# Kernel tuning notes

Measured on AMD Instinct MI355X. Metric: run time of the kernel, lower is better.

The kernel has to match this reference:

```python
import jax, jax.numpy as jnp
import numpy as np

B1, B2, N, D = 1, 128, 256, 256
H, C = 8, 32
OUT = 256


def setup_inputs() -> dict:
    key = jax.random.key(0)
    ks = jax.random.split(key, 8)
    in_data = jax.random.normal(ks[0], (B1, B2, N, D), dtype=jnp.float32)
    # binary mask, mostly unmasked
    mask = (jax.random.uniform(ks[1], (B1, B2, N)) > 0.1).astype(jnp.float32)
    nonbatched_bias = jax.random.normal(ks[2], (B1, H, N, N), dtype=jnp.float32)
    scale = 1.0 / np.sqrt(D)
    w_qkv = jax.random.normal(ks[3], (3 * H * C, D), dtype=jnp.float32) * scale  # torch Linear [out,in]
    w_gate = jax.random.normal(ks[4], (H * C, D), dtype=jnp.float32) * scale
    gating_bias = jnp.ones((H * C,), dtype=jnp.float32)
    w_o = jax.random.normal(ks[5], (OUT, H * C), dtype=jnp.float32) * scale
    b_o = jnp.zeros((OUT,), dtype=jnp.float32)
    return {
        "in_data": in_data,
        "mask": mask,
        "nonbatched_bias": nonbatched_bias,
        "w_qkv": w_qkv,
        "w_gate": w_gate,
        "gating_bias": gating_bias,
        "w_o": w_o,
        "b_o": b_o,
    }


def reference(in_data, mask, nonbatched_bias, w_qkv, w_gate, gating_bias, w_o, b_o):
    scaling = C ** (-0.5)
    # fused QKV projection (no bias): [b1,b2,n, 3*h*c]
    qkv = jnp.einsum("xynd,ed->xyne", in_data, w_qkv)
    q, k, v = jnp.split(qkv, 3, axis=-1)

    def heads(t):  # [b1,b2,n,h*c] -> [b1,b2,h,n,c]
        return t.reshape(B1, B2, N, H, C).transpose(0, 1, 3, 2, 4)

    q, k, v = heads(q) * scaling, heads(k), heads(v)
    logits = jnp.einsum("xyhqc,xyhkc->xyhqk", q, k)
    mask_bias = (1e9 * (mask - 1.0))[:, :, None, None, :]  # [b1,b2,1,1,n]
    logits = logits + mask_bias + nonbatched_bias[:, None]  # [b1,b2,h,q,k]
    weights = jax.nn.softmax(logits, axis=-1)
    wa = jnp.einsum("xyhqk,xyhkc->xyhqc", weights, v)
    wa = wa.transpose(0, 1, 3, 2, 4).reshape(B1, B2, N, H * C)
    # sigmoid gating: sigmoid(gate_linear(x) + gating_bias) * weighted_avg
    gate = jax.nn.sigmoid(jnp.einsum("xynd,ed->xyne", in_data, w_gate) + gating_bias)
    wa = gate * wa
    out = jnp.einsum("xyne,oe->xyno", wa, w_o) + b_o
    return out
```

## Files before the change

### kernel.cpp

```cpp
#include <hip/hip_runtime.h>
#include <stdint.h>

#define B2 128
#define NSEQ 256
#define DIM 256
#define NH 8
#define CH 32

typedef __attribute__((ext_vector_type(8))) __bf16 bf16x8;
typedef __attribute__((ext_vector_type(8))) unsigned short u16x8;
typedef __attribute__((ext_vector_type(4))) unsigned short u16x4;
typedef __attribute__((ext_vector_type(4))) float f32x4;

__device__ __forceinline__ unsigned short f2bf(float f) {
  unsigned int u = __builtin_bit_cast(unsigned int, f);
  u += 0x7FFFu + ((u >> 16) & 1u);
  return (unsigned short)(u >> 16);
}
__device__ __forceinline__ float bf2f(unsigned short h) {
  unsigned int u = ((unsigned int)h) << 16;
  return __builtin_bit_cast(float, u);
}
__device__ __forceinline__ bf16x8 as_bf(u16x8 v) { return __builtin_bit_cast(bf16x8, v); }

__device__ __forceinline__ void gload16(void* lds, const void* g) {
  __builtin_amdgcn_global_load_lds(
      (__attribute__((address_space(1))) void*)(g),
      (__attribute__((address_space(3))) void*)(lds), 16, 0, 0);
}

__global__ void k_convert(const float* __restrict__ x, const float* __restrict__ wqkv,
                          const float* __restrict__ wgate, const float* __restrict__ wo,
                          unsigned short* __restrict__ xb, unsigned short* __restrict__ wallb,
                          unsigned short* __restrict__ wob) {
  const int NX = 8388608, NWALL = 262144, NWO = 65536;
  int i = blockIdx.x * blockDim.x + threadIdx.x;
  int total4 = (NX + NWALL + NWO) >> 2;
  if (i >= total4) return;
  int e = i << 2;
  float4 v;
  unsigned short* dst;
  if (e < NX) {
    v = *reinterpret_cast<const float4*>(x + e);
    dst = xb + e;
  } else if (e < NX + NWALL) {
    int o = e - NX;
    v = (o < 196608) ? *reinterpret_cast<const float4*>(wqkv + o)
                     : *reinterpret_cast<const float4*>(wgate + (o - 196608));
    dst = wallb + o;
  } else {
    int o = e - NX - NWALL;
    v = *reinterpret_cast<const float4*>(wo + o);
    dst = wob + o;
  }
  u16x4 r;
  r[0] = f2bf(v.x); r[1] = f2bf(v.y); r[2] = f2bf(v.z); r[3] = f2bf(v.w);
  *reinterpret_cast<u16x4*>(dst) = r;
}

template <int MODE>
__launch_bounds__(256, 4)
__global__ void k_gemm(const unsigned short* __restrict__ A, const unsigned short* __restrict__ Bw,
                       unsigned short* __restrict__ qs, unsigned short* __restrict__ ksb,
                       unsigned short* __restrict__ vsb, unsigned short* __restrict__ gateb,
                       const float* __restrict__ gbias,
                       float* __restrict__ outp, const float* __restrict__ bo) {
  __shared__ __attribute__((aligned(16))) unsigned short As[2][4096];
  __shared__ __attribute__((aligned(16))) unsigned short Bs[2][4096];
  const int tid = threadIdx.x, lane = tid & 63, w = tid >> 6;
  const int wr = w >> 1, wc = w & 1;
  const int l15 = lane & 15, hi = lane >> 4;
  const int m0 = blockIdx.x * 128, n0 = blockIdx.y * 128;

  auto stage = [&](unsigned short* sbuf, const unsigned short* gsrc, int row0, int k0) {
#pragma unroll
    for (int q2 = 0; q2 < 2; ++q2) {
      int ob = (w * 2 + q2) * 1024 + (lane << 4);
      int r = ob >> 6, cb = ob & 63;
      int scb = cb ^ ((r & 3) << 4);
      const unsigned short* g = gsrc + (size_t)(row0 + r) * 256 + k0 + (scb >> 1);
      gload16(sbuf + (size_t)(w * 2 + q2) * 512, g);
    }
  };

  f32x4 acc[4][4];
#pragma unroll
  for (int i = 0; i < 4; ++i) {
#pragma unroll
    for (int j = 0; j < 4; ++j) acc[i][j] = (f32x4){0.f, 0.f, 0.f, 0.f};
  }

  stage(As[0], A, m0, 0);
  stage(Bs[0], Bw, n0, 0);
  asm volatile("s_waitcnt vmcnt(0)" ::: "memory");
  __syncthreads();

#pragma unroll
  for (int kt = 0; kt < 8; ++kt) {
    const int cur = kt & 1;
    if (kt < 7) {
      stage(As[cur ^ 1], A, m0, (kt + 1) * 32);
      stage(Bs[cur ^ 1], Bw, n0, (kt + 1) * 32);
    }
    {
      bf16x8 af[4], bfv[4];
      const int cbx = hi << 4;
#pragma unroll
      for (int fr = 0; fr < 4; ++fr) {
        int ra = wr * 64 + fr * 16 + l15;
        int off = ra * 64 + (cbx ^ ((ra & 3) << 4));
        af[fr] = *reinterpret_cast<const bf16x8*>((const char*)As[cur] + off);
      }
#pragma unroll
      for (int fc = 0; fc < 4; ++fc) {
        int rb = wc * 64 + fc * 16 + l15;
        int off = rb * 64 + (cbx ^ ((rb & 3) << 4));
        bfv[fc] = *reinterpret_cast<const bf16x8*>((const char*)Bs[cur] + off);
      }
#pragma unroll
      for (int fr = 0; fr < 4; ++fr) {
#pragma unroll
        for (int fc = 0; fc < 4; ++fc)
          acc[fr][fc] = __builtin_amdgcn_mfma_f32_16x16x32_bf16(af[fr], bfv[fc], acc[fr][fc], 0, 0, 0);
      }
    }
    asm volatile("s_waitcnt vmcnt(0)" ::: "memory");
    __syncthreads();
  }

  if (MODE == 0) {
#pragma unroll
    for (int fr = 0; fr < 4; ++fr) {
      int mrow = m0 + wr * 64 + fr * 16 + (hi << 2);
      int b = mrow >> 8, n = mrow & 255;
#pragma unroll
      for (int fc = 0; fc < 4; ++fc) {
        int e = n0 + wc * 64 + fc * 16 + l15;
        int which = e >> 8, loc = e & 255, hh = loc >> 5, cc = loc & 31;
#pragma unroll
        for (int i = 0; i < 4; ++i) {
          float v = acc[fr][fc][i];
          size_t idx = ((size_t)(b * 8 + hh) * 256 + (n + i)) * 32 + cc;
          if (which == 0) {
            qs[idx] = f2bf(v * 0.17677669529663687f);
          } else if (which == 1) {
            ksb[idx] = f2bf(v);
          } else if (which == 2) {
            vsb[idx] = f2bf(v);
          } else {
            float gsig = 1.0f / (1.0f + __expf(-(v + gbias[loc])));
            gateb[idx] = f2bf(gsig);
          }
        }
      }
    }
  } else {
#pragma unroll
    for (int fr = 0; fr < 4; ++fr) {
      int mrow = m0 + wr * 64 + fr * 16 + (hi << 2);
#pragma unroll
      for (int fc = 0; fc < 4; ++fc) {
        int e = n0 + wc * 64 + fc * 16 + l15;
        float bb = bo[e];
#pragma unroll
        for (int i = 0; i < 4; ++i)
          outp[(size_t)(mrow + i) * 256 + e] = acc[fr][fc][i] + bb;
      }
    }
  }
}

__launch_bounds__(256, 3)
__global__ void k_attn(const unsigned short* __restrict__ qs, const unsigned short* __restrict__ ksb,
                       const unsigned short* __restrict__ vsb, const unsigned short* __restrict__ gateb,
                       const float* __restrict__ mask, const float* __restrict__ nb,
                       unsigned short* __restrict__ wag) {
  __shared__ __attribute__((aligned(16))) unsigned short vt[32][264];
  __shared__ __attribute__((aligned(16))) unsigned short pch[4][16][72];
  __shared__ __attribute__((aligned(16))) unsigned short Kl[16][64][8];
  __shared__ __attribute__((aligned(16))) float mb[256];
  __shared__ float invl[4][16];
  const int tid = threadIdx.x, lane = tid & 63, w = tid >> 6;
  const int l15 = lane & 15, hi = lane >> 4;
  const int b = blockIdx.x, h = blockIdx.y, qz = blockIdx.z;
  const size_t bh = (size_t)(b * 8 + h);
  const unsigned short* kbase = ksb + bh * 8192;
  const unsigned short* vbase = vsb + bh * 8192;
  const unsigned short* qbase = qs + bh * 8192;
  const float* nbh = nb + (size_t)h * 65536;

  mb[tid] = 1e9f * (mask[b * 256 + tid] - 1.0f);
  {
    const unsigned short* vrow = vbase + tid * 32;
#pragma unroll
    for (int c0 = 0; c0 < 32; c0 += 8) {
      u16x8 vv = *reinterpret_cast<const u16x8*>(vrow + c0);
#pragma unroll
      for (int j = 0; j < 8; ++j) vt[c0 + j][tid] = vv[j];
    }
    const unsigned short* krow = kbase + tid * 32;
#pragma unroll
    for (int c8 = 0; c8 < 4; ++c8)
      *reinterpret_cast<u16x8*>(&Kl[tid >> 4][c8 * 16 + (tid & 15)][0]) =
          *reinterpret_cast<const u16x8*>(krow + c8 * 8);
  }
  __syncthreads();

  const f32x4 zero = {0.f, 0.f, 0.f, 0.f};
#pragma unroll 1
  for (int fr = 0; fr < 2; ++fr) {
    const int q0 = qz * 128 + w * 32 + fr * 16;
    u16x8 qf = *reinterpret_cast<const u16x8*>(qbase + (q0 + l15) * 32 + hi * 8);

    f32x4 sacc[16];
    __builtin_amdgcn_s_setprio(1);
#pragma unroll
    for (int kt = 0; kt < 16; ++kt) {
      bf16x8 kf = *reinterpret_cast<const bf16x8*>(&Kl[kt][lane][0]);
      sacc[kt] = __builtin_amdgcn_mfma_f32_16x16x32_bf16(kf, as_bf(qf), zero, 0, 0, 0);
    }
    __builtin_amdgcn_s_setprio(0);

    const float* nbq = nbh + (size_t)(q0 + l15) * 256;
#pragma unroll
    for (int kt = 0; kt < 16; ++kt) {
      float4 nb4 = *reinterpret_cast<const float4*>(nbq + kt * 16 + hi * 4);
      float4 mb4 = *reinterpret_cast<const float4*>(&mb[kt * 16 + hi * 4]);
      sacc[kt][0] += mb4.x + nb4.x;
      sacc[kt][1] += mb4.y + nb4.y;
      sacc[kt][2] += mb4.z + nb4.z;
      sacc[kt][3] += mb4.w + nb4.w;
    }
    float mx = -3.0e38f;
#pragma unroll
    for (int kt = 0; kt < 16; ++kt) {
#pragma unroll
      for (int i = 0; i < 4; ++i) mx = fmaxf(mx, sacc[kt][i]);
    }
    mx = fmaxf(mx, __shfl_xor(mx, 16));
    mx = fmaxf(mx, __shfl_xor(mx, 32));

    float sum = 0.f;
    f32x4 wacc[2];
    wacc[0] = zero; wacc[1] = zero;
#pragma unroll
    for (int c = 0; c < 4; ++c) {
#pragma unroll
      for (int ktl = 0; ktl < 4; ++ktl) {
        const int kt = c * 4 + ktl;
        u16x4 pv;
#pragma unroll
        for (int i = 0; i < 4; ++i) {
          float p = __expf(sacc[kt][i] - mx);
          sum += p;
          pv[i] = f2bf(p);
        }
        *reinterpret_cast<u16x4*>(&pch[w][l15][ktl * 16 + hi * 4]) = pv;
      }
      asm volatile("s_waitcnt lgkmcnt(0)" ::: "memory");
      __builtin_amdgcn_sched_barrier(0);
      __builtin_amdgcn_s_setprio(1);
#pragma unroll
      for (int ks2 = 0; ks2 < 2; ++ks2) {
        bf16x8 pa = *reinterpret_cast<const bf16x8*>(&pch[w][l15][ks2 * 32 + hi * 8]);
#pragma unroll
        for (int ct = 0; ct < 2; ++ct) {
          bf16x8 vb = *reinterpret_cast<const bf16x8*>(&vt[ct * 16 + l15][c * 64 + ks2 * 32 + hi * 8]);
          wacc[ct] = __builtin_amdgcn_mfma_f32_16x16x32_bf16(pa, vb, wacc[ct], 0, 0, 0);
        }
      }
      __builtin_amdgcn_s_setprio(0);
    }
    sum += __shfl_xor(sum, 16);
    sum += __shfl_xor(sum, 32);
    const float inv = 1.0f / sum;
    if (hi == 0) invl[w][l15] = inv;

    float* et = reinterpret_cast<float*>(&pch[w][0][0]);
#pragma unroll
    for (int ct = 0; ct < 2; ++ct) {
#pragma unroll
      for (int i = 0; i < 4; ++i)
        et[(hi * 4 + i) * 36 + ct * 16 + l15] = wacc[ct][i];
    }
    asm volatile("s_waitcnt lgkmcnt(0)" ::: "memory");
    __builtin_amdgcn_sched_barrier(0);
    const int eq = lane >> 2, eh = lane & 3;
    float4 v0 = *reinterpret_cast<const float4*>(&et[eq * 36 + eh * 8]);
    float4 v1 = *reinterpret_cast<const float4*>(&et[eq * 36 + eh * 8 + 4]);
    const float iv = invl[w][eq];
    const int qrow = q0 + eq;
    u16x8 g = *reinterpret_cast<const u16x8*>(gateb + bh * 8192 + qrow * 32 + eh * 8);
    u16x8 ov;
    ov[0] = f2bf(bf2f(g[0]) * v0.x * iv);
    ov[1] = f2bf(bf2f(g[1]) * v0.y * iv);
    ov[2] = f2bf(bf2f(g[2]) * v0.z * iv);
    ov[3] = f2bf(bf2f(g[3]) * v0.w * iv);
    ov[4] = f2bf(bf2f(g[4]) * v1.x * iv);
    ov[5] = f2bf(bf2f(g[5]) * v1.y * iv);
    ov[6] = f2bf(bf2f(g[6]) * v1.z * iv);
    ov[7] = f2bf(bf2f(g[7]) * v1.w * iv);
    *reinterpret_cast<u16x8*>(wag + ((size_t)(b * 256 + qrow)) * 256 + h * 32 + eh * 8) = ov;
    asm volatile("s_waitcnt lgkmcnt(0)" ::: "memory");
    __builtin_amdgcn_sched_barrier(0);
  }
}

extern "C" void kernel_launch(void* const* d_in, const int* in_sizes, int n_in,
                              void* d_out, int out_size, void* d_ws, size_t ws_size,
                              hipStream_t stream) {
  const float* x     = (const float*)d_in[0];
  const float* mask  = (const float*)d_in[1];
  const float* nb    = (const float*)d_in[2];
  const float* wqkv  = (const float*)d_in[3];
  const float* wgate = (const float*)d_in[4];
  const float* gbias = (const float*)d_in[5];
  const float* wo    = (const float*)d_in[6];
  const float* bo    = (const float*)d_in[7];
  float* outp = (float*)d_out;

  char* ws = (char*)d_ws;
  unsigned short* xb    = (unsigned short*)(ws);
  unsigned short* wallb = (unsigned short*)(ws + 16777216);
  unsigned short* wob   = (unsigned short*)(ws + 17301504);
  unsigned short* qs    = (unsigned short*)(ws + 17432576);
  unsigned short* ksb   = (unsigned short*)(ws + 34209792);
  unsigned short* vsb   = (unsigned short*)(ws + 50987008);
  unsigned short* gateb = (unsigned short*)(ws + 67764224);
  unsigned short* wag   = xb;

  k_convert<<<dim3(8512), dim3(256), 0, stream>>>(x, wqkv, wgate, wo, xb, wallb, wob);
  k_gemm<0><<<dim3(256, 8), dim3(256), 0, stream>>>(xb, wallb, qs, ksb, vsb, gateb, gbias, nullptr, nullptr);
  k_attn<<<dim3(128, 8, 2), dim3(256), 0, stream>>>(qs, ksb, vsb, gateb, mask, nb, wag);
  k_gemm<1><<<dim3(256, 2), dim3(256), 0, stream>>>(wag, wob, nullptr, nullptr, nullptr, nullptr, nullptr, outp, bo);
}
```

Measured before the change: 132.7 us.

## Fuse fp32-to-bf16 input conversion into QKV GEMM and merge attention query halves

The QKV/gate GEMM now stages fp32 activations directly into LDS and converts them to bf16 with packed cvt instructions while building fragments. This removes the separate conversion pass over the 8M-element input, which cost one full read and one write. The attention kernel now uses 512-thread blocks that cover all 256 queries of a (batch, head) pair, so K and V are loaded and transposed once instead of twice. In exchange the GEMM reads twice the bytes per A tile, uses more LDS (occupancy hint lowered to 3), and attention blocks are larger with fewer of them.

```diff
diff --git a/kernel.cpp b/kernel.cpp
--- a/kernel.cpp
+++ b/kernel.cpp
@@ -10,6 +10,7 @@
 typedef __attribute__((ext_vector_type(8))) __bf16 bf16x8;
 typedef __attribute__((ext_vector_type(8))) unsigned short u16x8;
 typedef __attribute__((ext_vector_type(4))) unsigned short u16x4;
+typedef __attribute__((ext_vector_type(4))) unsigned int u32x4;
 typedef __attribute__((ext_vector_type(4))) float f32x4;
 
 __device__ __forceinline__ unsigned short f2bf(float f) {
@@ -22,6 +23,11 @@
   return __builtin_bit_cast(float, u);
 }
 __device__ __forceinline__ bf16x8 as_bf(u16x8 v) { return __builtin_bit_cast(bf16x8, v); }
+__device__ __forceinline__ unsigned int cvtpk(float lo, float hi) {
+  unsigned int r;
+  asm("v_cvt_pk_bf16_f32 %0, %1, %2" : "=v"(r) : "v"(lo), "v"(hi));
+  return r;
+}
 
 __device__ __forceinline__ void gload16(void* lds, const void* g) {
   __builtin_amdgcn_global_load_lds(
@@ -29,27 +35,22 @@
       (__attribute__((address_space(3))) void*)(lds), 16, 0, 0);
 }
 
-__global__ void k_convert(const float* __restrict__ x, const float* __restrict__ wqkv,
-                          const float* __restrict__ wgate, const float* __restrict__ wo,
-                          unsigned short* __restrict__ xb, unsigned short* __restrict__ wallb,
-                          unsigned short* __restrict__ wob) {
-  const int NX = 8388608, NWALL = 262144, NWO = 65536;
+__global__ void k_convert(const float* __restrict__ wqkv, const float* __restrict__ wgate,
+                          const float* __restrict__ wo,
+                          unsigned short* __restrict__ wallb, unsigned short* __restrict__ wob) {
+  const int NWALL = 262144, NWO = 65536;
   int i = blockIdx.x * blockDim.x + threadIdx.x;
-  int total4 = (NX + NWALL + NWO) >> 2;
+  int total4 = (NWALL + NWO) >> 2;
   if (i >= total4) return;
   int e = i << 2;
   float4 v;
   unsigned short* dst;
-  if (e < NX) {
-    v = *reinterpret_cast<const float4*>(x + e);
-    dst = xb + e;
-  } else if (e < NX + NWALL) {
-    int o = e - NX;
-    v = (o < 196608) ? *reinterpret_cast<const float4*>(wqkv + o)
-                     : *reinterpret_cast<const float4*>(wgate + (o - 196608));
-    dst = wallb + o;
+  if (e < NWALL) {
+    v = (e < 196608) ? *reinterpret_cast<const float4*>(wqkv + e)
+                     : *reinterpret_cast<const float4*>(wgate + (e - 196608));
+    dst = wallb + e;
   } else {
-    int o = e - NX - NWALL;
+    int o = e - NWALL;
     v = *reinterpret_cast<const float4*>(wo + o);
     dst = wob + o;
   }
@@ -59,27 +60,49 @@
 }
 
 template <int MODE>
-__launch_bounds__(256, 4)
-__global__ void k_gemm(const unsigned short* __restrict__ A, const unsigned short* __restrict__ Bw,
+__launch_bounds__(256, MODE == 0 ? 3 : 4)
+__global__ void k_gemm(const float* __restrict__ Af, const unsigned short* __restrict__ Ab,
+                       const unsigned short* __restrict__ Bw,
                        unsigned short* __restrict__ qs, unsigned short* __restrict__ ksb,
                        unsigned short* __restrict__ vsb, unsigned short* __restrict__ gateb,
                        const float* __restrict__ gbias,
                        float* __restrict__ outp, const float* __restrict__ bo) {
-  __shared__ __attribute__((aligned(16))) unsigned short As[2][4096];
+  __shared__ __attribute__((aligned(16))) char As[2][MODE == 0 ? 16384 : 8192];
   __shared__ __attribute__((aligned(16))) unsigned short Bs[2][4096];
   const int tid = threadIdx.x, lane = tid & 63, w = tid >> 6;
   const int wr = w >> 1, wc = w & 1;
   const int l15 = lane & 15, hi = lane >> 4;
   const int m0 = blockIdx.x * 128, n0 = blockIdx.y * 128;
 
-  auto stage = [&](unsigned short* sbuf, const unsigned short* gsrc, int row0, int k0) {
+  auto stageA = [&](int buf, int k0) {
+    if constexpr (MODE == 0) {
+#pragma unroll
+      for (int q2 = 0; q2 < 4; ++q2) {
+        int ob = (w * 4 + q2) * 1024 + (lane << 4);
+        int r = ob >> 7, cb = ob & 127;
+        int scb = cb ^ ((r & 7) << 4);
+        const float* g = Af + (size_t)(m0 + r) * 256 + k0 + (scb >> 2);
+        gload16(As[buf] + (size_t)(w * 4 + q2) * 1024, g);
+      }
+    } else {
+#pragma unroll
+      for (int q2 = 0; q2 < 2; ++q2) {
+        int ob = (w * 2 + q2) * 1024 + (lane << 4);
+        int r = ob >> 6, cb = ob & 63;
+        int scb = cb ^ ((r & 3) << 4);
+        const unsigned short* g = Ab + (size_t)(m0 + r) * 256 + k0 + (scb >> 1);
+        gload16(As[buf] + (size_t)(w * 2 + q2) * 1024, g);
+      }
+    }
+  };
+  auto stageB = [&](int buf, int k0) {
 #pragma unroll
     for (int q2 = 0; q2 < 2; ++q2) {
       int ob = (w * 2 + q2) * 1024 + (lane << 4);
       int r = ob >> 6, cb = ob & 63;
       int scb = cb ^ ((r & 3) << 4);
-      const unsigned short* g = gsrc + (size_t)(row0 + r) * 256 + k0 + (scb >> 1);
-      gload16(sbuf + (size_t)(w * 2 + q2) * 512, g);
+      const unsigned short* g = Bw + (size_t)(n0 + r) * 256 + k0 + (scb >> 1);
+      gload16((char*)Bs[buf] + (size_t)(w * 2 + q2) * 1024, g);
     }
   };
 
@@ -90,8 +113,8 @@
     for (int j = 0; j < 4; ++j) acc[i][j] = (f32x4){0.f, 0.f, 0.f, 0.f};
   }
 
-  stage(As[0], A, m0, 0);
-  stage(Bs[0], Bw, n0, 0);
+  stageA(0, 0);
+  stageB(0, 0);
   asm volatile("s_waitcnt vmcnt(0)" ::: "memory");
   __syncthreads();
 
@@ -99,22 +122,34 @@
   for (int kt = 0; kt < 8; ++kt) {
     const int cur = kt & 1;
     if (kt < 7) {
-      stage(As[cur ^ 1], A, m0, (kt + 1) * 32);
-      stage(Bs[cur ^ 1], Bw, n0, (kt + 1) * 32);
+      stageA(cur ^ 1, (kt + 1) * 32);
+      stageB(cur ^ 1, (kt + 1) * 32);
     }
     {
       bf16x8 af[4], bfv[4];
-      const int cbx = hi << 4;
 #pragma unroll
       for (int fr = 0; fr < 4; ++fr) {
         int ra = wr * 64 + fr * 16 + l15;
-        int off = ra * 64 + (cbx ^ ((ra & 3) << 4));
-        af[fr] = *reinterpret_cast<const bf16x8*>((const char*)As[cur] + off);
+        if constexpr (MODE == 0) {
+          const char* base = As[cur] + ra * 128;
+          int sw = (ra & 7) << 4;
+          f32x4 a0 = *reinterpret_cast<const f32x4*>(base + ((hi * 32) ^ sw));
+          f32x4 a1 = *reinterpret_cast<const f32x4*>(base + ((hi * 32 + 16) ^ sw));
+          u32x4 afu;
+          afu[0] = cvtpk(a0[0], a0[1]);
+          afu[1] = cvtpk(a0[2], a0[3]);
+          afu[2] = cvtpk(a1[0], a1[1]);
+          afu[3] = cvtpk(a1[2], a1[3]);
+          af[fr] = __builtin_bit_cast(bf16x8, afu);
+        } else {
+          int off = ra * 64 + ((hi << 4) ^ ((ra & 3) << 4));
+          af[fr] = *reinterpret_cast<const bf16x8*>(As[cur] + off);
+        }
       }
 #pragma unroll
       for (int fc = 0; fc < 4; ++fc) {
         int rb = wc * 64 + fc * 16 + l15;
-        int off = rb * 64 + (cbx ^ ((rb & 3) << 4));
+        int off = rb * 64 + ((hi << 4) ^ ((rb & 3) << 4));
         bfv[fc] = *reinterpret_cast<const bf16x8*>((const char*)Bs[cur] + off);
       }
 #pragma unroll
@@ -170,27 +205,27 @@
   }
 }
 
-__launch_bounds__(256, 3)
+__launch_bounds__(512, 6)
 __global__ void k_attn(const unsigned short* __restrict__ qs, const unsigned short* __restrict__ ksb,
                        const unsigned short* __restrict__ vsb, const unsigned short* __restrict__ gateb,
                        const float* __restrict__ mask, const float* __restrict__ nb,
                        unsigned short* __restrict__ wag) {
   __shared__ __attribute__((aligned(16))) unsigned short vt[32][264];
-  __shared__ __attribute__((aligned(16))) unsigned short pch[4][16][72];
+  __shared__ __attribute__((aligned(16))) unsigned short pch[8][16][72];
   __shared__ __attribute__((aligned(16))) unsigned short Kl[16][64][8];
   __shared__ __attribute__((aligned(16))) float mb[256];
-  __shared__ float invl[4][16];
+  __shared__ float invl[8][16];
   const int tid = threadIdx.x, lane = tid & 63, w = tid >> 6;
   const int l15 = lane & 15, hi = lane >> 4;
-  const int b = blockIdx.x, h = blockIdx.y, qz = blockIdx.z;
+  const int b = blockIdx.x, h = blockIdx.y;
   const size_t bh = (size_t)(b * 8 + h);
   const unsigned short* kbase = ksb + bh * 8192;
   const unsigned short* vbase = vsb + bh * 8192;
   const unsigned short* qbase = qs + bh * 8192;
   const float* nbh = nb + (size_t)h * 65536;
 
-  mb[tid] = 1e9f * (mask[b * 256 + tid] - 1.0f);
-  {
+  if (tid < 256) {
+    mb[tid] = 1e9f * (mask[b * 256 + tid] - 1.0f);
     const unsigned short* vrow = vbase + tid * 32;
 #pragma unroll
     for (int c0 = 0; c0 < 32; c0 += 8) {
@@ -198,10 +233,12 @@
 #pragma unroll
       for (int j = 0; j < 8; ++j) vt[c0 + j][tid] = vv[j];
     }
-    const unsigned short* krow = kbase + tid * 32;
+  } else {
+    const int key = tid - 256;
+    const unsigned short* krow = kbase + key * 32;
 #pragma unroll
     for (int c8 = 0; c8 < 4; ++c8)
-      *reinterpret_cast<u16x8*>(&Kl[tid >> 4][c8 * 16 + (tid & 15)][0]) =
+      *reinterpret_cast<u16x8*>(&Kl[key >> 4][c8 * 16 + (key & 15)][0]) =
           *reinterpret_cast<const u16x8*>(krow + c8 * 8);
   }
   __syncthreads();
@@ -209,7 +246,7 @@
   const f32x4 zero = {0.f, 0.f, 0.f, 0.f};
 #pragma unroll 1
   for (int fr = 0; fr < 2; ++fr) {
-    const int q0 = qz * 128 + w * 32 + fr * 16;
+    const int q0 = w * 32 + fr * 16;
     u16x8 qf = *reinterpret_cast<const u16x8*>(qbase + (q0 + l15) * 32 + hi * 8);
 
     f32x4 sacc[16];
@@ -320,17 +357,16 @@
   float* outp = (float*)d_out;
 
   char* ws = (char*)d_ws;
-  unsigned short* xb    = (unsigned short*)(ws);
+  unsigned short* wag   = (unsigned short*)(ws);
   unsigned short* wallb = (unsigned short*)(ws + 16777216);
   unsigned short* wob   = (unsigned short*)(ws + 17301504);
   unsigned short* qs    = (unsigned short*)(ws + 17432576);
   unsigned short* ksb   = (unsigned short*)(ws + 34209792);
   unsigned short* vsb   = (unsigned short*)(ws + 50987008);
   unsigned short* gateb = (unsigned short*)(ws + 67764224);
-  unsigned short* wag   = xb;
-
-  k_convert<<<dim3(8512), dim3(256), 0, stream>>>(x, wqkv, wgate, wo, xb, wallb, wob);
-  k_gemm<0><<<dim3(256, 8), dim3(256), 0, stream>>>(xb, wallb, qs, ksb, vsb, gateb, gbias, nullptr, nullptr);
-  k_attn<<<dim3(128, 8, 2), dim3(256), 0, stream>>>(qs, ksb, vsb, gateb, mask, nb, wag);
-  k_gemm<1><<<dim3(256, 2), dim3(256), 0, stream>>>(wag, wob, nullptr, nullptr, nullptr, nullptr, nullptr, outp, bo);
-}
+
+  k_convert<<<dim3(320), dim3(256), 0, stream>>>(wqkv, wgate, wo, wallb, wob);
+  k_gemm<0><<<dim3(256, 8), dim3(256), 0, stream>>>(x, nullptr, wallb, qs, ksb, vsb, gateb, gbias, nullptr, nullptr);
+  k_attn<<<dim3(128, 8), dim3(512), 0, stream>>>(qs, ksb, vsb, gateb, mask, nb, wag);
+  k_gemm<1><<<dim3(256, 2), dim3(256), 0, stream>>>(nullptr, wag, wob, nullptr, nullptr, nullptr, nullptr, nullptr, outp, bo);
+}
```

New measurement: 158.3 us. 1.19x slower.

## Widen QKV GEMM tiles, merge attention query halves, restructure LDS swizzle and barriers

Applied to the files above, without the earlier changes.

The QKV/gate projection GEMM becomes a 512-thread kernel with 128x256 tiles, so each A tile is reused across more output columns. Both GEMMs switch to a new paired-row XOR swizzle for LDS staging and issue the next stage's loads only after a single barrier per k-step. The attention kernel now covers all 256 queries per (batch, head) with 8 waves instead of two blocks, which halves the redundant K/V staging. Several explicit lgkmcnt waits and sched barriers are replaced with plain compiler memory fences; this relies on the compiler to insert LDS waits correctly and lowers attention occupancy.

```diff
diff --git a/kernel.cpp b/kernel.cpp
--- a/kernel.cpp
+++ b/kernel.cpp
@@ -10,6 +10,7 @@
 typedef __attribute__((ext_vector_type(8))) __bf16 bf16x8;
 typedef __attribute__((ext_vector_type(8))) unsigned short u16x8;
 typedef __attribute__((ext_vector_type(4))) unsigned short u16x4;
+typedef __attribute__((ext_vector_type(4))) unsigned int u32x4;
 typedef __attribute__((ext_vector_type(4))) float f32x4;
 
 __device__ __forceinline__ unsigned short f2bf(float f) {
@@ -58,28 +59,132 @@
   *reinterpret_cast<u16x4*>(dst) = r;
 }
 
-template <int MODE>
+__launch_bounds__(512, 4)
+__global__ void k_gemm0(const unsigned short* __restrict__ Ab, const unsigned short* __restrict__ Bw,
+                        unsigned short* __restrict__ qs, unsigned short* __restrict__ ksb,
+                        unsigned short* __restrict__ vsb, unsigned short* __restrict__ gateb,
+                        const float* __restrict__ gbias) {
+  __shared__ __attribute__((aligned(16))) char As[2][8192];
+  __shared__ __attribute__((aligned(16))) char Bs[2][16384];
+  const int tid = threadIdx.x, lane = tid & 63, w = tid >> 6;
+  const int wr = w >> 2, wc = w & 3;
+  const int l15 = lane & 15, hi = lane >> 4;
+  const int m0 = blockIdx.x * 128, n0 = blockIdx.y * 256;
+
+  auto stageA = [&](int buf, int k0) {
+    int i = tid;
+    int rp = i >> 3, sp = i & 7;
+    int sl = sp ^ (rp & 7);
+    int row = 2 * rp + (sl >> 2), s3 = sl & 3;
+    const unsigned short* g = Ab + (size_t)(m0 + row) * 256 + k0 + s3 * 8;
+    gload16(As[buf] + w * 1024, g);
+  };
+  auto stageB = [&](int buf, int k0) {
+#pragma unroll
+    for (int q2 = 0; q2 < 2; ++q2) {
+      int i = q2 * 512 + tid;
+      int rp = i >> 3, sp = i & 7;
+      int sl = sp ^ (rp & 7);
+      int row = 2 * rp + (sl >> 2), s3 = sl & 3;
+      const unsigned short* g = Bw + (size_t)(n0 + row) * 256 + k0 + s3 * 8;
+      gload16(Bs[buf] + q2 * 8192 + w * 1024, g);
+    }
+  };
+
+  f32x4 acc[4][4];
+#pragma unroll
+  for (int i = 0; i < 4; ++i) {
+#pragma unroll
+    for (int j = 0; j < 4; ++j) acc[i][j] = (f32x4){0.f, 0.f, 0.f, 0.f};
+  }
+
+  stageA(0, 0);
+  stageB(0, 0);
+
+#pragma unroll
+  for (int kt = 0; kt < 8; ++kt) {
+    const int cur = kt & 1;
+    asm volatile("s_waitcnt vmcnt(0)" ::: "memory");
+    __builtin_amdgcn_sched_barrier(0);
+    __builtin_amdgcn_s_barrier();
+    __builtin_amdgcn_sched_barrier(0);
+    if (kt < 7) {
+      stageA(cur ^ 1, (kt + 1) * 32);
+      stageB(cur ^ 1, (kt + 1) * 32);
+    }
+    {
+      bf16x8 af[4], bfv[4];
+#pragma unroll
+      for (int fr = 0; fr < 4; ++fr) {
+        int ra = wr * 64 + fr * 16 + l15;
+        int rp = ra >> 1;
+        int sl = ((ra & 1) << 2) | hi;
+        int off = rp * 128 + (sl ^ (rp & 7)) * 16;
+        af[fr] = *reinterpret_cast<const bf16x8*>(As[cur] + off);
+      }
+#pragma unroll
+      for (int fc = 0; fc < 4; ++fc) {
+        int rb = wc * 64 + fc * 16 + l15;
+        int rp = rb >> 1;
+        int sl = ((rb & 1) << 2) | hi;
+        int off = rp * 128 + (sl ^ (rp & 7)) * 16;
+        bfv[fc] = *reinterpret_cast<const bf16x8*>(Bs[cur] + off);
+      }
+#pragma unroll
+      for (int fr = 0; fr < 4; ++fr) {
+#pragma unroll
+        for (int fc = 0; fc < 4; ++fc)
+          acc[fr][fc] = __builtin_amdgcn_mfma_f32_16x16x32_bf16(af[fr], bfv[fc], acc[fr][fc], 0, 0, 0);
+      }
+    }
+  }
+
+#pragma unroll
+  for (int fr = 0; fr < 4; ++fr) {
+    int mrow = m0 + wr * 64 + fr * 16 + (hi << 2);
+    int b = mrow >> 8, n = mrow & 255;
+#pragma unroll
+    for (int fc = 0; fc < 4; ++fc) {
+      int e = n0 + wc * 64 + fc * 16 + l15;
+      int which = e >> 8, loc = e & 255, hh = loc >> 5, cc = loc & 31;
+#pragma unroll
+      for (int i = 0; i < 4; ++i) {
+        float v = acc[fr][fc][i];
+        size_t idx = ((size_t)(b * 8 + hh) * 256 + (n + i)) * 32 + cc;
+        if (which == 0) {
+          qs[idx] = f2bf(v * 0.17677669529663687f);
+        } else if (which == 1) {
+          ksb[idx] = f2bf(v);
+        } else if (which == 2) {
+          vsb[idx] = f2bf(v);
+        } else {
+          float gsig = 1.0f / (1.0f + __expf(-(v + gbias[loc])));
+          gateb[idx] = f2bf(gsig);
+        }
+      }
+    }
+  }
+}
+
 __launch_bounds__(256, 4)
-__global__ void k_gemm(const unsigned short* __restrict__ A, const unsigned short* __restrict__ Bw,
-                       unsigned short* __restrict__ qs, unsigned short* __restrict__ ksb,
-                       unsigned short* __restrict__ vsb, unsigned short* __restrict__ gateb,
-                       const float* __restrict__ gbias,
-                       float* __restrict__ outp, const float* __restrict__ bo) {
-  __shared__ __attribute__((aligned(16))) unsigned short As[2][4096];
-  __shared__ __attribute__((aligned(16))) unsigned short Bs[2][4096];
+__global__ void k_gemm1(const unsigned short* __restrict__ Ab, const unsigned short* __restrict__ Bw,
+                        float* __restrict__ outp, const float* __restrict__ bo) {
+  __shared__ __attribute__((aligned(16))) char As[2][8192];
+  __shared__ __attribute__((aligned(16))) char Bs[2][8192];
   const int tid = threadIdx.x, lane = tid & 63, w = tid >> 6;
   const int wr = w >> 1, wc = w & 1;
   const int l15 = lane & 15, hi = lane >> 4;
   const int m0 = blockIdx.x * 128, n0 = blockIdx.y * 128;
 
-  auto stage = [&](unsigned short* sbuf, const unsigned short* gsrc, int row0, int k0) {
+  auto stage_pair = [&](char* sbuf, const unsigned short* gsrc, int row0, int k0) {
 #pragma unroll
     for (int q2 = 0; q2 < 2; ++q2) {
-      int ob = (w * 2 + q2) * 1024 + (lane << 4);
-      int r = ob >> 6, cb = ob & 63;
-      int scb = cb ^ ((r & 3) << 4);
-      const unsigned short* g = gsrc + (size_t)(row0 + r) * 256 + k0 + (scb >> 1);
-      gload16(sbuf + (size_t)(w * 2 + q2) * 512, g);
+      int i = q2 * 256 + tid;
+      int rp = i >> 3, sp = i & 7;
+      int sl = sp ^ (rp & 7);
+      int row = 2 * rp + (sl >> 2), s3 = sl & 3;
+      const unsigned short* g = gsrc + (size_t)(row0 + row) * 256 + k0 + s3 * 8;
+      gload16(sbuf + q2 * 4096 + w * 1024, g);
     }
   };
 
@@ -90,32 +195,37 @@
     for (int j = 0; j < 4; ++j) acc[i][j] = (f32x4){0.f, 0.f, 0.f, 0.f};
   }
 
-  stage(As[0], A, m0, 0);
-  stage(Bs[0], Bw, n0, 0);
-  asm volatile("s_waitcnt vmcnt(0)" ::: "memory");
-  __syncthreads();
+  stage_pair(As[0], Ab, m0, 0);
+  stage_pair(Bs[0], Bw, n0, 0);
 
 #pragma unroll
   for (int kt = 0; kt < 8; ++kt) {
     const int cur = kt & 1;
+    asm volatile("s_waitcnt vmcnt(0)" ::: "memory");
+    __builtin_amdgcn_sched_barrier(0);
+    __builtin_amdgcn_s_barrier();
+    __builtin_amdgcn_sched_barrier(0);
     if (kt < 7) {
-      stage(As[cur ^ 1], A, m0, (kt + 1) * 32);
-      stage(Bs[cur ^ 1], Bw, n0, (kt + 1) * 32);
+      stage_pair(As[cur ^ 1], Ab, m0, (kt + 1) * 32);
+      stage_pair(Bs[cur ^ 1], Bw, n0, (kt + 1) * 32);
     }
     {
       bf16x8 af[4], bfv[4];
-      const int cbx = hi << 4;
 #pragma unroll
       for (int fr = 0; fr < 4; ++fr) {
         int ra = wr * 64 + fr * 16 + l15;
-        int off = ra * 64 + (cbx ^ ((ra & 3) << 4));
-        af[fr] = *reinterpret_cast<const bf16x8*>((const char*)As[cur] + off);
+        int rp = ra >> 1;
+        int sl = ((ra & 1) << 2) | hi;
+        int off = rp * 128 + (sl ^ (rp & 7)) * 16;
+        af[fr] = *reinterpret_cast<const bf16x8*>(As[cur] + off);
       }
 #pragma unroll
       for (int fc = 0; fc < 4; ++fc) {
         int rb = wc * 64 + fc * 16 + l15;
-        int off = rb * 64 + (cbx ^ ((rb & 3) << 4));
-        bfv[fc] = *reinterpret_cast<const bf16x8*>((const char*)Bs[cur] + off);
+        int rp = rb >> 1;
+        int sl = ((rb & 1) << 2) | hi;
+        int off = rp * 128 + (sl ^ (rp & 7)) * 16;
+        bfv[fc] = *reinterpret_cast<const bf16x8*>(Bs[cur] + off);
       }
 #pragma unroll
       for (int fr = 0; fr < 4; ++fr) {
@@ -124,73 +234,43 @@
           acc[fr][fc] = __builtin_amdgcn_mfma_f32_16x16x32_bf16(af[fr], bfv[fc], acc[fr][fc], 0, 0, 0);
       }
     }
-    asm volatile("s_waitcnt vmcnt(0)" ::: "memory");
-    __syncthreads();
-  }
-
-  if (MODE == 0) {
-#pragma unroll
-    for (int fr = 0; fr < 4; ++fr) {
-      int mrow = m0 + wr * 64 + fr * 16 + (hi << 2);
-      int b = mrow >> 8, n = mrow & 255;
-#pragma unroll
-      for (int fc = 0; fc < 4; ++fc) {
-        int e = n0 + wc * 64 + fc * 16 + l15;
-        int which = e >> 8, loc = e & 255, hh = loc >> 5, cc = loc & 31;
-#pragma unroll
-        for (int i = 0; i < 4; ++i) {
-          float v = acc[fr][fc][i];
-          size_t idx = ((size_t)(b * 8 + hh) * 256 + (n + i)) * 32 + cc;
-          if (which == 0) {
-            qs[idx] = f2bf(v * 0.17677669529663687f);
-          } else if (which == 1) {
-            ksb[idx] = f2bf(v);
-          } else if (which == 2) {
-            vsb[idx] = f2bf(v);
-          } else {
-            float gsig = 1.0f / (1.0f + __expf(-(v + gbias[loc])));
-            gateb[idx] = f2bf(gsig);
-          }
-        }
-      }
-    }
-  } else {
-#pragma unroll
-    for (int fr = 0; fr < 4; ++fr) {
-      int mrow = m0 + wr * 64 + fr * 16 + (hi << 2);
-#pragma unroll
-      for (int fc = 0; fc < 4; ++fc) {
-        int e = n0 + wc * 64 + fc * 16 + l15;
-        float bb = bo[e];
-#pragma unroll
-        for (int i = 0; i < 4; ++i)
-          outp[(size_t)(mrow + i) * 256 + e] = acc[fr][fc][i] + bb;
-      }
-    }
-  }
-}
-
-__launch_bounds__(256, 3)
+  }
+
+#pragma unroll
+  for (int fr = 0; fr < 4; ++fr) {
+    int mrow = m0 + wr * 64 + fr * 16 + (hi << 2);
+#pragma unroll
+    for (int fc = 0; fc < 4; ++fc) {
+      int e = n0 + wc * 64 + fc * 16 + l15;
+      float bb = bo[e];
+#pragma unroll
+      for (int i = 0; i < 4; ++i)
+        outp[(size_t)(mrow + i) * 256 + e] = acc[fr][fc][i] + bb;
+    }
+  }
+}
+
+__launch_bounds__(512, 2)
 __global__ void k_attn(const unsigned short* __restrict__ qs, const unsigned short* __restrict__ ksb,
                        const unsigned short* __restrict__ vsb, const unsigned short* __restrict__ gateb,
                        const float* __restrict__ mask, const float* __restrict__ nb,
                        unsigned short* __restrict__ wag) {
   __shared__ __attribute__((aligned(16))) unsigned short vt[32][264];
-  __shared__ __attribute__((aligned(16))) unsigned short pch[4][16][72];
+  __shared__ __attribute__((aligned(16))) unsigned short pch[8][16][72];
   __shared__ __attribute__((aligned(16))) unsigned short Kl[16][64][8];
   __shared__ __attribute__((aligned(16))) float mb[256];
-  __shared__ float invl[4][16];
+  __shared__ float invl[8][16];
   const int tid = threadIdx.x, lane = tid & 63, w = tid >> 6;
   const int l15 = lane & 15, hi = lane >> 4;
-  const int b = blockIdx.x, h = blockIdx.y, qz = blockIdx.z;
+  const int b = blockIdx.x, h = blockIdx.y;
   const size_t bh = (size_t)(b * 8 + h);
   const unsigned short* kbase = ksb + bh * 8192;
   const unsigned short* vbase = vsb + bh * 8192;
   const unsigned short* qbase = qs + bh * 8192;
   const float* nbh = nb + (size_t)h * 65536;
 
-  mb[tid] = 1e9f * (mask[b * 256 + tid] - 1.0f);
-  {
+  if (tid < 256) {
+    mb[tid] = 1e9f * (mask[b * 256 + tid] - 1.0f);
     const unsigned short* vrow = vbase + tid * 32;
 #pragma unroll
     for (int c0 = 0; c0 < 32; c0 += 8) {
@@ -198,10 +278,12 @@
 #pragma unroll
       for (int j = 0; j < 8; ++j) vt[c0 + j][tid] = vv[j];
     }
-    const unsigned short* krow = kbase + tid * 32;
+  } else {
+    const int key = tid - 256;
+    const unsigned short* krow = kbase + key * 32;
 #pragma unroll
     for (int c8 = 0; c8 < 4; ++c8)
-      *reinterpret_cast<u16x8*>(&Kl[tid >> 4][c8 * 16 + (tid & 15)][0]) =
+      *reinterpret_cast<u16x8*>(&Kl[key >> 4][c8 * 16 + (key & 15)][0]) =
           *reinterpret_cast<const u16x8*>(krow + c8 * 8);
   }
   __syncthreads();
@@ -209,7 +291,7 @@
   const f32x4 zero = {0.f, 0.f, 0.f, 0.f};
 #pragma unroll 1
   for (int fr = 0; fr < 2; ++fr) {
-    const int q0 = qz * 128 + w * 32 + fr * 16;
+    const int q0 = w * 32 + fr * 16;
     u16x8 qf = *reinterpret_cast<const u16x8*>(qbase + (q0 + l15) * 32 + hi * 8);
 
     f32x4 sacc[16];
@@ -257,8 +339,7 @@
         }
         *reinterpret_cast<u16x4*>(&pch[w][l15][ktl * 16 + hi * 4]) = pv;
       }
-      asm volatile("s_waitcnt lgkmcnt(0)" ::: "memory");
-      __builtin_amdgcn_sched_barrier(0);
+      asm volatile("" ::: "memory");
       __builtin_amdgcn_s_setprio(1);
 #pragma unroll
       for (int ks2 = 0; ks2 < 2; ++ks2) {
@@ -276,6 +357,7 @@
     const float inv = 1.0f / sum;
     if (hi == 0) invl[w][l15] = inv;
 
+    asm volatile("" ::: "memory");
     float* et = reinterpret_cast<float*>(&pch[w][0][0]);
 #pragma unroll
     for (int ct = 0; ct < 2; ++ct) {
@@ -283,8 +365,7 @@
       for (int i = 0; i < 4; ++i)
         et[(hi * 4 + i) * 36 + ct * 16 + l15] = wacc[ct][i];
     }
-    asm volatile("s_waitcnt lgkmcnt(0)" ::: "memory");
-    __builtin_amdgcn_sched_barrier(0);
+    asm volatile("" ::: "memory");
     const int eq = lane >> 2, eh = lane & 3;
     float4 v0 = *reinterpret_cast<const float4*>(&et[eq * 36 + eh * 8]);
     float4 v1 = *reinterpret_cast<const float4*>(&et[eq * 36 + eh * 8 + 4]);
@@ -301,8 +382,7 @@
     ov[6] = f2bf(bf2f(g[6]) * v1.z * iv);
     ov[7] = f2bf(bf2f(g[7]) * v1.w * iv);
     *reinterpret_cast<u16x8*>(wag + ((size_t)(b * 256 + qrow)) * 256 + h * 32 + eh * 8) = ov;
-    asm volatile("s_waitcnt lgkmcnt(0)" ::: "memory");
-    __builtin_amdgcn_sched_barrier(0);
+    asm volatile("" ::: "memory");
   }
 }
 
@@ -330,7 +410,7 @@
   unsigned short* wag   = xb;
 
   k_convert<<<dim3(8512), dim3(256), 0, stream>>>(x, wqkv, wgate, wo, xb, wallb, wob);
-  k_gemm<0><<<dim3(256, 8), dim3(256), 0, stream>>>(xb, wallb, qs, ksb, vsb, gateb, gbias, nullptr, nullptr);
-  k_attn<<<dim3(128, 8, 2), dim3(256), 0, stream>>>(qs, ksb, vsb, gateb, mask, nb, wag);
-  k_gemm<1><<<dim3(256, 2), dim3(256), 0, stream>>>(wag, wob, nullptr, nullptr, nullptr, nullptr, nullptr, outp, bo);
-}
+  k_gemm0<<<dim3(256, 4), dim3(512), 0, stream>>>(xb, wallb, qs, ksb, vsb, gateb, gbias);
+  k_attn<<<dim3(128, 8), dim3(512), 0, stream>>>(qs, ksb, vsb, gateb, mask, nb, wag);
+  k_gemm1<<<dim3(256, 2), dim3(256), 0, stream>>>(wag, wob, outp, bo);
+}
```

Result: faster. 121.9 us (-8.2%).
